# Kernel tuning notes

Hardware: AMD Instinct MI355X
Metric: run time of the kernel (lower is better)

Reference implementation:

```python
import jax, jax.numpy as jnp
import numpy as np

RADIUS = 3
DIAM = 2 * RADIUS + 1  # 7
NP = DIAM * DIAM       # 49 taps


def _cubic(d, a=-0.75):
    # torch bicubic kernel (a = -0.75)
    d = np.abs(d)
    return np.where(d <= 1, (a + 2) * d**3 - (a + 3) * d**2 + 1,
                    np.where(d < 2, a * d**3 - 5 * a * d**2 + 8 * a * d - 4 * a, 0.0))


def _resize_matrix(out_size, in_size):
    # dense [out,in] matrix reproducing torch F.interpolate bicubic, align_corners=False
    i = np.arange(out_size)
    x = (i + 0.5) * in_size / out_size - 0.5
    x0 = np.floor(x).astype(np.int64)
    t = x - x0
    W = np.zeros((out_size, in_size), np.float32)
    for k in range(-1, 3):
        w = _cubic(t - k)
        idx = np.clip(x0 + k, 0, in_size - 1)  # border replicate
        np.add.at(W, (i, idx), w.astype(np.float32))
    return jnp.asarray(W)


def _bicubic(x, GH, GW):
    B, C, H, W = x.shape
    Wh = _resize_matrix(GH, H)
    Ww = _resize_matrix(GW, W)
    return jnp.einsum('Hh,bchw,Ww->bcHW', Wh, x, Ww)


def _jbu(source, guidance, w1, b1, w2, b2, temp, sigma):
    # FeatUp JBULearnedRange.forward (eval mode: Dropout2d is identity)
    B, _, GH, GW = guidance.shape
    # range_proj: 1x1 conv -> GELU -> 1x1 conv
    q = jnp.einsum('kc,bchw->bkhw', w1, guidance) + b1[None, :, None, None]
    q = jax.nn.gelu(q, approximate=False)
    q = jnp.einsum('kc,bchw->bkhw', w2, q) + b2[None, :, None, None]  # [B,32,GH,GW]
    qp = jnp.pad(q, ((0, 0), (0, 0), (RADIUS, RADIUS), (RADIUS, RADIUS)), mode='reflect')
    # scores[b,p,h,w] = <key at center, key at offset p> (avoids B*32*49*H*W unfold)
    scores = jnp.stack([jnp.sum(qp[:, :, di:di + GH, dj:dj + GW] * q, axis=1)
                        for di in range(DIAM) for dj in range(DIAM)], axis=1)  # [B,49,GH,GW]
    t = jnp.clip(jnp.exp(temp), 1e-4, 1e4)
    range_kernel = jax.nn.softmax(t * scores, axis=1)
    dist = jnp.linspace(-1.0, 1.0, DIAM)
    gy, gx = jnp.meshgrid(dist, dist, indexing='ij')
    spatial_kernel = jnp.exp(-(gy**2 + gx**2) / (2.0 * sigma**2)).reshape(1, NP, 1, 1)
    k = range_kernel * spatial_kernel
    k = k / jnp.clip(jnp.sum(k, axis=1, keepdims=True), 1e-7, None)
    hr = _bicubic(source, GH, GW)
    hrp = jnp.pad(hr, ((0, 0), (0, 0), (RADIUS, RADIUS), (RADIUS, RADIUS)), mode='reflect')
    # AdaptiveConv: per-pixel 7x7 kernel applied to all channels
    out = jnp.zeros_like(hr)
    p_idx = 0
    for di in range(DIAM):
        for dj in range(DIAM):
            out = out + hrp[:, :, di:di + GH, dj:dj + GW] * k[:, p_idx][:, None]
            p_idx += 1
    return out


def _forward(x, guidance, linear_w, linear_b, w1s, b1s, w2s, b2s, temps, sigmas):
    f = (x @ linear_w.T + linear_b).reshape(-1, 3, 18, 18)
    for i in range(4):  # up1..up4, each fed the FULL guidance as in the Decoder
        f = _jbu(f, guidance, w1s[i], b1s[i], w2s[i], b2s[i], temps[i], sigmas[i])
    return f


def setup_inputs() -> dict:
    key = jax.random.key(0)
    ks = jax.random.split(key, 6)
    B = 8
    return {
        'x': jax.random.normal(ks[0], (B, 1000), jnp.float32),
        'guidance': jax.random.uniform(ks[1], (B, 3, 224, 224), jnp.float32),
        'linear_w': jax.random.normal(ks[2], (972, 1000), jnp.float32) * 0.03,
        'linear_b': jnp.zeros((972,), jnp.float32),
        'w1s': jax.random.normal(ks[3], (4, 32, 3), jnp.float32) * 0.1,
        'b1s': jnp.zeros((4, 32), jnp.float32),
        'w2s': jax.random.normal(ks[4], (4, 32, 32), jnp.float32) * 0.1,
        'b2s': jnp.zeros((4, 32), jnp.float32),
        'temps': jnp.zeros((4,), jnp.float32),   # range_temp init 0.0
        'sigmas': jnp.ones((4,), jnp.float32),   # sigma_spatial init 1.0
    }


def reference(x, guidance, linear_w, linear_b, w1s, b1s, w2s, b2s, temps, sigmas):
    return _forward(x, guidance, linear_w, linear_b, w1s, b1s, w2s, b2s, temps, sigmas)
```

## Files before the change

kernel.cpp:

```cpp
#include <hip/hip_runtime.h>
#include <hip/hip_fp16.h>
#include <math.h>

#define GHH 224
#define GWW 224
#define HW (GHH*GWW)
#define BATCH 8
#define RAD 3
#define DIAM 7
#define QC 32
#define TILE 16
#define TP (TILE + 2*RAD)
#define TPIX (TP*TP)
#define CS 485

#define HRH_COLS 24
#define PSTR (TP*HRH_COLS)
#define HRH_B (8*PSTR*2)
#define SMEM_B (HRH_B + 4*CS*16)

#define L2E 1.44269504f

typedef _Float16 h2 __attribute__((ext_vector_type(2)));
typedef _Float16 v8h __attribute__((ext_vector_type(8)));
typedef float v4f __attribute__((ext_vector_type(4)));

__device__ __forceinline__ int refl(int i) {
    if (i < 0) i = -i;
    if (i >= GHH) i = 2 * GHH - 2 - i;
    return i;
}

__device__ __forceinline__ float gelu_fast(float v) {
    float u = 0.7978845608f * v * (1.f + 0.044715f * v * v);
    float e = __builtin_amdgcn_exp2f(u * (2.f * L2E));
    float th = 1.f - 2.f / (e + 1.f);
    return 0.5f * v * (1.f + th);
}

__global__ void linear_prep_kernel(const float* __restrict__ x,
                                   const float* __restrict__ W,
                                   const float* __restrict__ bias,
                                   float* __restrict__ f0,
                                   const float* __restrict__ w2s,
                                   __half* __restrict__ wsB,
                                   const float* __restrict__ w1s,
                                   const float* __restrict__ b1s,
                                   __half* __restrict__ wsW1,
                                   const float* __restrict__ guid,
                                   float4* __restrict__ guid4) {
    int blk = blockIdx.x;
    if (blk >= 1946) {
        int i = (blk - 1946) * 256 + threadIdx.x;
        int b = i / HW, pix = i % HW;
        guid4[i] = make_float4(guid[(b * 3) * HW + pix],
                               guid[(b * 3 + 1) * HW + pix],
                               guid[(b * 3 + 2) * HW + pix], 0.f);
        return;
    }
    if (blk == 1945) {
        int tid = threadIdx.x;
        if (tid < 128) {
            int s = tid >> 5, c = tid & 31;
            wsW1[tid * 4 + 0] = __float2half(w1s[s * 96 + c * 3 + 0]);
            wsW1[tid * 4 + 1] = __float2half(w1s[s * 96 + c * 3 + 1]);
            wsW1[tid * 4 + 2] = __float2half(w1s[s * 96 + c * 3 + 2]);
            wsW1[tid * 4 + 3] = __float2half(b1s[s * 32 + c]);
        }
        return;
    }
    if (blk == 1944) {
        int tid = threadIdx.x;
        int s = tid >> 6, l = tid & 63;
        int n0 = l & 15, kq = l >> 4;
        const float* w2 = w2s + s * 1024;
        __half* dst = wsB + (size_t)tid * 16;
        #pragma unroll
        for (int j = 0; j < 8; j++) {
            dst[j]     = __float2half(w2[n0 * QC + kq * 8 + j]);
            dst[8 + j] = __float2half(w2[(n0 + 16) * QC + kq * 8 + j]);
        }
        return;
    }
    int gwave = (blk * blockDim.x + threadIdx.x) >> 6;
    int lane = threadIdx.x & 63;
    if (gwave >= BATCH * 972) return;
    int b = gwave / 972, j = gwave % 972;
    const float* xr = x + b * 1000;
    const float* wr = W + j * 1000;
    float s = 0.f;
    for (int k = lane; k < 1000; k += 64)
        s += xr[k] * wr[k];
    #pragma unroll
    for (int off = 32; off; off >>= 1) s += __shfl_down(s, off, 64);
    if (lane == 0) f0[gwave] = s + bias[j];
}

__device__ __forceinline__ float cubicw(float d) {
    d = fabsf(d);
    if (d <= 1.f) return ((1.25f * d - 2.25f) * d) * d + 1.f;
    if (d < 2.f)  return ((-0.75f * d + 3.75f) * d - 6.f) * d + 3.f;
    return 0.f;
}

__global__ void bicubic_kernel(const float* __restrict__ f0, float4* __restrict__ hr4) {
    int idx = blockIdx.x * blockDim.x + threadIdx.x;
    if (idx >= BATCH * HW) return;
    int pix = idx % HW;
    int b = idx / HW;
    int w = pix % GWW, h = pix / GWW;
    float xx = (w + 0.5f) * (18.f / 224.f) - 0.5f;
    float yy = (h + 0.5f) * (18.f / 224.f) - 0.5f;
    float fx0 = floorf(xx), fy0 = floorf(yy);
    int x0 = (int)fx0, y0 = (int)fy0;
    float tx = xx - fx0, ty = yy - fy0;
    float wx[4], wy[4];
    int ix[4], iy[4];
    #pragma unroll
    for (int k = 0; k < 4; k++) {
        wx[k] = cubicw(tx - (float)(k - 1));
        wy[k] = cubicw(ty - (float)(k - 1));
        int a = x0 + (k - 1); ix[k] = min(max(a, 0), 17);
        a = y0 + (k - 1);     iy[k] = min(max(a, 0), 17);
    }
    float acc[3];
    #pragma unroll
    for (int c = 0; c < 3; c++) {
        const float* src = f0 + (b * 3 + c) * 324;
        float a = 0.f;
        #pragma unroll
        for (int ky = 0; ky < 4; ky++) {
            float rowv = 0.f;
            #pragma unroll
            for (int kx = 0; kx < 4; kx++) rowv += wx[kx] * src[iy[ky] * 18 + ix[kx]];
            a += wy[ky] * rowv;
        }
        acc[c] = a;
    }
    hr4[idx] = make_float4(acc[0], acc[1], acc[2], 0.f);
}

__global__ __launch_bounds__(256, 4) void jbu_kernel(
    const float4* __restrict__ guid4,
    const __half* __restrict__ wsW1,
    const __half* __restrict__ wsB, const float* __restrict__ b2,
    const float4* __restrict__ hr4,
    float4* __restrict__ out4,
    float* __restrict__ outP,
    const float* __restrict__ temps,
    const float* __restrict__ sigmas,
    int stage)
{
    __shared__ __align__(16) char smem[SMEM_B];
    _Float16* hrh = (_Float16*)smem;
    char* sqb = smem + HRH_B;

    const int tx = threadIdx.x, ty = threadIdx.y;
    const int tid = ty * TILE + tx;
    const int b = blockIdx.z;
    const int h0 = blockIdx.y * TILE, w0 = blockIdx.x * TILE;

    for (int i = tid; i < TPIX; i += 256) {
        int r = i / TP, cx = i % TP;
        int gh = refl(h0 - RAD + r), gw = refl(w0 - RAD + cx);
        float4 v = hr4[(size_t)b * HW + (size_t)gh * GWW + gw];
        _Float16 hx = (_Float16)v.x, hy = (_Float16)v.y, hz = (_Float16)v.z;
        int base = r * HRH_COLS + cx;
        hrh[0 * PSTR + base] = hx;
        hrh[1 * PSTR + base] = hy;
        hrh[2 * PSTR + base] = hz;
        hrh[3 * PSTR + base] = (_Float16)1.0f;
        hrh[4 * PSTR + base] = (_Float16)(v.x - (float)hx);
        hrh[5 * PSTR + base] = (_Float16)(v.y - (float)hy);
        hrh[6 * PSTR + base] = (_Float16)(v.z - (float)hz);
        hrh[7 * PSTR + base] = (_Float16)0.0f;
    }
    for (int i = tid; i < 8 * TP * 2; i += 256) {
        int p = i / (TP * 2), rem = i % (TP * 2);
        int r = rem >> 1, cc = 22 + (rem & 1);
        hrh[p * PSTR + r * HRH_COLS + cc] = (_Float16)0.0f;
    }

    const int w = tid >> 6, l = tid & 63;
    const int n0 = l & 15, kq = l >> 4;
    const v8h* Bp = (const v8h*)(wsB + ((size_t)stage * 64 + l) * 16);
    const v8h W2a = Bp[0], W2b = Bp[1];
    const float4 b2a = *(const float4*)(b2 + 4 * kq);
    const float4 b2b = *(const float4*)(b2 + 16 + 4 * kq);
    union { _Float16 h[32]; float4 f4[4]; } W1;
    {
        const float4* wp = (const float4*)(wsW1 + stage * 128 + kq * 32);
        W1.f4[0] = wp[0]; W1.f4[1] = wp[1]; W1.f4[2] = wp[2]; W1.f4[3] = wp[3];
    }
    const int plane0 = kq >> 1;
    const int boff   = (kq & 1) * 8;

    #pragma unroll 1
    for (int r2 = 0; r2 < 2; r2++) {
        #pragma unroll
        for (int tt = 0; tt < 4; tt++) {
            int base = r2 * 256 + w * 64 + tt * 16;
            int p = base + n0;
            int pc = min(p, TPIX - 1);
            int rr = pc / TP, cc = pc - rr * TP;
            int gh = refl(h0 - RAD + rr), gw = refl(w0 - RAD + cc);
            float4 g = guid4[(size_t)b * HW + (size_t)gh * GWW + gw];
            union { _Float16 h[8]; v8h v; } A;
            #pragma unroll
            for (int j = 0; j < 8; j++) {
                float vv = fmaf((float)W1.h[j * 4], g.x,
                           fmaf((float)W1.h[j * 4 + 1], g.y,
                           fmaf((float)W1.h[j * 4 + 2], g.z, (float)W1.h[j * 4 + 3])));
                A.h[j] = (_Float16)gelu_fast(vv);
            }
            v4f D0 = {0.f, 0.f, 0.f, 0.f}, D1 = {0.f, 0.f, 0.f, 0.f};
            D0 = __builtin_amdgcn_mfma_f32_16x16x32_f16(W2a, A.v, D0, 0, 0, 0);
            D1 = __builtin_amdgcn_mfma_f32_16x16x32_f16(W2b, A.v, D1, 0, 0, 0);
            if (p < TPIX) {
                union { _Float16 h[4]; uint2 u; } q0, q1;
                q0.h[0] = (_Float16)(D0[0] + b2a.x);
                q0.h[1] = (_Float16)(D0[1] + b2a.y);
                q0.h[2] = (_Float16)(D0[2] + b2a.z);
                q0.h[3] = (_Float16)(D0[3] + b2a.w);
                q1.h[0] = (_Float16)(D1[0] + b2b.x);
                q1.h[1] = (_Float16)(D1[1] + b2b.y);
                q1.h[2] = (_Float16)(D1[2] + b2b.z);
                q1.h[3] = (_Float16)(D1[3] + b2b.w);
                *(uint2*)(sqb + (plane0 * CS + p) * 16 + boff)       = q0.u;
                *(uint2*)(sqb + ((2 + plane0) * CS + p) * 16 + boff) = q1.u;
            }
        }
    }
    __syncthreads();

    const int wv = tid >> 6;
    const int g = l >> 4, c = l & 15;

    float t = __expf(temps[stage]);
    t = fminf(fmaxf(t, 1e-4f), 1e4f);
    const float tl2 = t * L2E;
    float sig = sigmas[stage];
    float inv2s2 = 1.f / (2.f * sig * sig);
    float sdv[DIAM];
    #pragma unroll
    for (int i = 0; i < DIAM; i++) {
        float d = (float)(i - 3) * (1.f / 3.f);
        sdv[i] = __expf(-d * d * inv2s2);
    }
    float lc2[8];
    #pragma unroll
    for (int jj = 0; jj < 8; jj++) {
        int dj = 8 * g + jj - c;
        float d = (float)(dj - 3) * (1.f / 3.f);
        lc2[jj] = (dj >= 0 && dj <= 6) ? (-d * d * inv2s2 * L2E) : -1.44e38f;
    }
    const int nbb = 8 * (c >> 2) + (c & 3);
    const int nb0 = min(nbb, 21);
    const int nb1 = min(nbb + 4, 21);
    const int pA = c & 3;

    #pragma unroll 2
    for (int rr = 0; rr < 4; rr++) {
        const int row = wv * 4 + rr;
        const v8h Bc = *(const v8h*)(sqb + (size_t)(g * CS + (row + RAD) * TP + RAD + c) * 16);
        v4f D2 = {0.f, 0.f, 0.f, 0.f};
        #pragma unroll
        for (int di = 0; di < DIAM; di++) {
            const int prow = row + di;
            const v8h A0 = *(const v8h*)(sqb + (size_t)(g * CS + prow * TP + nb0) * 16);
            const v8h A1 = *(const v8h*)(sqb + (size_t)(g * CS + prow * TP + nb1) * 16);
            v4f S0 = {0.f, 0.f, 0.f, 0.f}, S1 = {0.f, 0.f, 0.f, 0.f};
            S0 = __builtin_amdgcn_mfma_f32_16x16x32_f16(A0, Bc, S0, 0, 0, 0);
            S1 = __builtin_amdgcn_mfma_f32_16x16x32_f16(A1, Bc, S1, 0, 0, 0);
            const float sy = sdv[di];
            union { _Float16 h[8]; v8h v; } Wg;
            #pragma unroll
            for (int j = 0; j < 4; j++) {
                Wg.h[j]     = (_Float16)(__builtin_amdgcn_exp2f(fmaf(S0[j], tl2, lc2[j])) * sy);
                Wg.h[4 + j] = (_Float16)(__builtin_amdgcn_exp2f(fmaf(S1[j], tl2, lc2[4 + j])) * sy);
            }
            const v8h Hh = *(const v8h*)(smem + (size_t)((pA * TP + prow) * HRH_COLS + 8 * g) * 2);
            const v8h Hl = *(const v8h*)(smem + (size_t)(((pA + 4) * TP + prow) * HRH_COLS + 8 * g) * 2);
            D2 = __builtin_amdgcn_mfma_f32_16x16x32_f16(Hh, Wg.v, D2, 0, 0, 0);
            D2 = __builtin_amdgcn_mfma_f32_16x16x32_f16(Hl, Wg.v, D2, 0, 0, 0);
        }
        if (l < 16) {
            float rk = 1.f / fmaxf(D2[3], 1e-7f);
            if (stage < 3) {
                out4[(size_t)b * HW + (size_t)(h0 + row) * GWW + (w0 + c)] =
                    make_float4(D2[0] * rk, D2[1] * rk, D2[2] * rk, 0.f);
            } else {
                size_t obase = (size_t)b * 3 * HW + (size_t)(h0 + row) * GWW + (w0 + c);
                outP[obase]          = D2[0] * rk;
                outP[obase + HW]     = D2[1] * rk;
                outP[obase + 2 * HW] = D2[2] * rk;
            }
        }
    }
}

extern "C" void kernel_launch(void* const* d_in, const int* in_sizes, int n_in,
                              void* d_out, int out_size, void* d_ws, size_t ws_size,
                              hipStream_t stream) {
    const float* x      = (const float*)d_in[0];
    const float* guid   = (const float*)d_in[1];
    const float* lw     = (const float*)d_in[2];
    const float* lb     = (const float*)d_in[3];
    const float* w1s    = (const float*)d_in[4];
    const float* b1s    = (const float*)d_in[5];
    const float* w2s    = (const float*)d_in[6];
    const float* b2s    = (const float*)d_in[7];
    const float* temps  = (const float*)d_in[8];
    const float* sigmas = (const float*)d_in[9];

    char* ws = (char*)d_ws;
    const size_t P4_BYTES = (size_t)BATCH * HW * sizeof(float4);
    float4* guid4 = (float4*)ws;
    float4* hr4A  = (float4*)(ws + P4_BYTES);
    float4* hr4B  = (float4*)(ws + 2 * P4_BYTES);
    float*  f0    = (float*)(ws + 3 * P4_BYTES);
    __half* wsB   = (__half*)(ws + 3 * P4_BYTES + 31104);
    __half* wsW1  = (__half*)(ws + 3 * P4_BYTES + 31104 + 8192);

    linear_prep_kernel<<<1946 + 1568, 256, 0, stream>>>(
        x, lw, lb, f0, w2s, wsB, w1s, b1s, wsW1, guid, guid4);
    bicubic_kernel<<<(BATCH * HW + 255) / 256, 256, 0, stream>>>(f0, hr4A);

    dim3 jgrid(14, 14, BATCH), jblock(16, 16);
    const float4* hins[4]  = { hr4A, hr4B, hr4A, hr4B };
    float4*       fouts[4] = { hr4B, hr4A, hr4B, nullptr };
    for (int s = 0; s < 4; s++) {
        jbu_kernel<<<jgrid, jblock, 0, stream>>>(
            guid4, wsW1, wsB, b2s + s * 32,
            hins[s], fouts[s], (s == 3) ? (float*)d_out : nullptr,
            temps, sigmas, s);
    }
}
```

Baseline: 292.5 us.

## Split range-projection into a separate kernel writing q image to global memory

Moves the per-pixel range projection (1x1 conv, GELU, MFMA 1x1 conv) out of the JBU kernel into a new q_kernel that writes a half-precision 32-channel q image to workspace once per stage. The JBU kernel then loads the haloed q tile from global memory instead of recomputing it, which removes the redundant halo recomputation (484 vs 256 pixels per tile). The cost is an extra kernel launch per stage and about 4x64B of global traffic per pixel written and then re-read with halo. The score loop unroll is also reduced from 2 to 1.

```diff
diff --git a/kernel.cpp b/kernel.cpp
--- a/kernel.cpp
+++ b/kernel.cpp
@@ -140,10 +140,64 @@
     hr4[idx] = make_float4(acc[0], acc[1], acc[2], 0.f);
 }
 
-__global__ __launch_bounds__(256, 4) void jbu_kernel(
+__global__ __launch_bounds__(256) void q_kernel(
     const float4* __restrict__ guid4,
     const __half* __restrict__ wsW1,
     const __half* __restrict__ wsB, const float* __restrict__ b2,
+    float4* __restrict__ qimg,
+    int stage)
+{
+    const int tid = threadIdx.x;
+    const int l = tid & 63;
+    const int gw = (blockIdx.x * 256 + tid) >> 6;
+    const int n0 = l & 15, kq = l >> 4;
+    const int b = gw / 392;
+    const int pix0 = (gw - b * 392) * 128;
+
+    const v8h* Bp = (const v8h*)(wsB + ((size_t)stage * 64 + l) * 16);
+    const v8h W2a = Bp[0], W2b = Bp[1];
+    const float4 b2a = *(const float4*)(b2 + 4 * kq);
+    const float4 b2b = *(const float4*)(b2 + 16 + 4 * kq);
+    union { _Float16 h[32]; float4 f4[4]; } W1;
+    {
+        const float4* wp = (const float4*)(wsW1 + stage * 128 + kq * 32);
+        W1.f4[0] = wp[0]; W1.f4[1] = wp[1]; W1.f4[2] = wp[2]; W1.f4[3] = wp[3];
+    }
+    const int plane0 = kq >> 1;
+    const int boff   = (kq & 1) * 8;
+    char* qc = (char*)qimg;
+
+    #pragma unroll 1
+    for (int it = 0; it < 8; it++) {
+        int pix = pix0 + it * 16 + n0;
+        float4 g = guid4[(size_t)b * HW + pix];
+        union { _Float16 h[8]; v8h v; } A;
+        #pragma unroll
+        for (int j = 0; j < 8; j++) {
+            float vv = fmaf((float)W1.h[j * 4], g.x,
+                       fmaf((float)W1.h[j * 4 + 1], g.y,
+                       fmaf((float)W1.h[j * 4 + 2], g.z, (float)W1.h[j * 4 + 3])));
+            A.h[j] = (_Float16)gelu_fast(vv);
+        }
+        v4f D0 = {0.f, 0.f, 0.f, 0.f}, D1 = {0.f, 0.f, 0.f, 0.f};
+        D0 = __builtin_amdgcn_mfma_f32_16x16x32_f16(W2a, A.v, D0, 0, 0, 0);
+        D1 = __builtin_amdgcn_mfma_f32_16x16x32_f16(W2b, A.v, D1, 0, 0, 0);
+        union { _Float16 h[4]; uint2 u; } q0, q1;
+        q0.h[0] = (_Float16)(D0[0] + b2a.x);
+        q0.h[1] = (_Float16)(D0[1] + b2a.y);
+        q0.h[2] = (_Float16)(D0[2] + b2a.z);
+        q0.h[3] = (_Float16)(D0[3] + b2a.w);
+        q1.h[0] = (_Float16)(D1[0] + b2b.x);
+        q1.h[1] = (_Float16)(D1[1] + b2b.y);
+        q1.h[2] = (_Float16)(D1[2] + b2b.z);
+        q1.h[3] = (_Float16)(D1[3] + b2b.w);
+        *(uint2*)(qc + ((size_t)(b * 4 + plane0) * HW + pix) * 16 + boff)     = q0.u;
+        *(uint2*)(qc + ((size_t)(b * 4 + 2 + plane0) * HW + pix) * 16 + boff) = q1.u;
+    }
+}
+
+__global__ __launch_bounds__(256, 4) void jbu_kernel(
+    const float4* __restrict__ qimg,
     const float4* __restrict__ hr4,
     float4* __restrict__ out4,
     float* __restrict__ outP,
@@ -154,16 +208,24 @@
     __shared__ __align__(16) char smem[SMEM_B];
     _Float16* hrh = (_Float16*)smem;
     char* sqb = smem + HRH_B;
+    float4* sqf4 = (float4*)sqb;
 
     const int tx = threadIdx.x, ty = threadIdx.y;
     const int tid = ty * TILE + tx;
     const int b = blockIdx.z;
     const int h0 = blockIdx.y * TILE, w0 = blockIdx.x * TILE;
 
+    const float4* qb = qimg + (size_t)b * 4 * HW;
+    const float4* hb = hr4 + (size_t)b * HW;
     for (int i = tid; i < TPIX; i += 256) {
         int r = i / TP, cx = i % TP;
         int gh = refl(h0 - RAD + r), gw = refl(w0 - RAD + cx);
-        float4 v = hr4[(size_t)b * HW + (size_t)gh * GWW + gw];
+        size_t gpix = (size_t)gh * GWW + gw;
+        sqf4[i]          = qb[gpix];
+        sqf4[CS + i]     = qb[HW + gpix];
+        sqf4[2 * CS + i] = qb[2 * HW + gpix];
+        sqf4[3 * CS + i] = qb[3 * HW + gpix];
+        float4 v = hb[gpix];
         _Float16 hx = (_Float16)v.x, hy = (_Float16)v.y, hz = (_Float16)v.z;
         int base = r * HRH_COLS + cx;
         hrh[0 * PSTR + base] = hx;
@@ -180,60 +242,10 @@
         int r = rem >> 1, cc = 22 + (rem & 1);
         hrh[p * PSTR + r * HRH_COLS + cc] = (_Float16)0.0f;
     }
-
-    const int w = tid >> 6, l = tid & 63;
-    const int n0 = l & 15, kq = l >> 4;
-    const v8h* Bp = (const v8h*)(wsB + ((size_t)stage * 64 + l) * 16);
-    const v8h W2a = Bp[0], W2b = Bp[1];
-    const float4 b2a = *(const float4*)(b2 + 4 * kq);
-    const float4 b2b = *(const float4*)(b2 + 16 + 4 * kq);
-    union { _Float16 h[32]; float4 f4[4]; } W1;
-    {
-        const float4* wp = (const float4*)(wsW1 + stage * 128 + kq * 32);
-        W1.f4[0] = wp[0]; W1.f4[1] = wp[1]; W1.f4[2] = wp[2]; W1.f4[3] = wp[3];
-    }
-    const int plane0 = kq >> 1;
-    const int boff   = (kq & 1) * 8;
-
-    #pragma unroll 1
-    for (int r2 = 0; r2 < 2; r2++) {
-        #pragma unroll
-        for (int tt = 0; tt < 4; tt++) {
-            int base = r2 * 256 + w * 64 + tt * 16;
-            int p = base + n0;
-            int pc = min(p, TPIX - 1);
-            int rr = pc / TP, cc = pc - rr * TP;
-            int gh = refl(h0 - RAD + rr), gw = refl(w0 - RAD + cc);
-            float4 g = guid4[(size_t)b * HW + (size_t)gh * GWW + gw];
-            union { _Float16 h[8]; v8h v; } A;
-            #pragma unroll
-            for (int j = 0; j < 8; j++) {
-                float vv = fmaf((float)W1.h[j * 4], g.x,
-                           fmaf((float)W1.h[j * 4 + 1], g.y,
-                           fmaf((float)W1.h[j * 4 + 2], g.z, (float)W1.h[j * 4 + 3])));
-                A.h[j] = (_Float16)gelu_fast(vv);
-            }
-            v4f D0 = {0.f, 0.f, 0.f, 0.f}, D1 = {0.f, 0.f, 0.f, 0.f};
-            D0 = __builtin_amdgcn_mfma_f32_16x16x32_f16(W2a, A.v, D0, 0, 0, 0);
-            D1 = __builtin_amdgcn_mfma_f32_16x16x32_f16(W2b, A.v, D1, 0, 0, 0);
-            if (p < TPIX) {
-                union { _Float16 h[4]; uint2 u; } q0, q1;
-                q0.h[0] = (_Float16)(D0[0] + b2a.x);
-                q0.h[1] = (_Float16)(D0[1] + b2a.y);
-                q0.h[2] = (_Float16)(D0[2] + b2a.z);
-                q0.h[3] = (_Float16)(D0[3] + b2a.w);
-                q1.h[0] = (_Float16)(D1[0] + b2b.x);
-                q1.h[1] = (_Float16)(D1[1] + b2b.y);
-                q1.h[2] = (_Float16)(D1[2] + b2b.z);
-                q1.h[3] = (_Float16)(D1[3] + b2b.w);
-                *(uint2*)(sqb + (plane0 * CS + p) * 16 + boff)       = q0.u;
-                *(uint2*)(sqb + ((2 + plane0) * CS + p) * 16 + boff) = q1.u;
-            }
-        }
-    }
     __syncthreads();
 
     const int wv = tid >> 6;
+    const int l = tid & 63;
     const int g = l >> 4, c = l & 15;
 
     float t = __expf(temps[stage]);
@@ -259,7 +271,7 @@
     const int nb1 = min(nbb + 4, 21);
     const int pA = c & 3;
 
-    #pragma unroll 2
+    #pragma unroll 1
     for (int rr = 0; rr < 4; rr++) {
         const int row = wv * 4 + rr;
         const v8h Bc = *(const v8h*)(sqb + (size_t)(g * CS + (row + RAD) * TP + RAD + c) * 16);
@@ -321,6 +333,7 @@
     float*  f0    = (float*)(ws + 3 * P4_BYTES);
     __half* wsB   = (__half*)(ws + 3 * P4_BYTES + 31104);
     __half* wsW1  = (__half*)(ws + 3 * P4_BYTES + 31104 + 8192);
+    float4* qimg  = (float4*)(ws + 3 * P4_BYTES + 40320);
 
     linear_prep_kernel<<<1946 + 1568, 256, 0, stream>>>(
         x, lw, lb, f0, w2s, wsB, w1s, b1s, wsW1, guid, guid4);
@@ -330,9 +343,9 @@
     const float4* hins[4]  = { hr4A, hr4B, hr4A, hr4B };
     float4*       fouts[4] = { hr4B, hr4A, hr4B, nullptr };
     for (int s = 0; s < 4; s++) {
+        q_kernel<<<784, 256, 0, stream>>>(guid4, wsW1, wsB, b2s + s * 32, qimg, s);
         jbu_kernel<<<jgrid, jblock, 0, stream>>>(
-            guid4, wsW1, wsB, b2s + s * 32,
-            hins[s], fouts[s], (s == 3) ? (float*)d_out : nullptr,
+            qimg, hins[s], fouts[s], (s == 3) ? (float*)d_out : nullptr,
             temps, sigmas, s);
     }
 }
```

Measured after the change: 279.2 us. 4.6% less time.
